# Optimization experiments

Measured on AMD Instinct MI355X. Metric: run time of the kernel, lower is better.

## Reference

```python
import jax, jax.numpy as jnp
import numpy as np
import math

B, C, IMG, P = 32, 3, 224, 16
E, DEPTH, H, MLP = 768, 12, 12, 3072
NP = (IMG // P) ** 2          # 196 patches
S = NP + 1                    # 197 tokens with cls
NCLS = 10
HD = E // H                   # 64 head dim
EPS = 1e-5


def setup_inputs() -> dict:
    key = jax.random.key(0)
    ks = iter(jax.random.split(key, 64))
    n = lambda shape, s=0.02: (jax.random.normal(next(ks), shape, jnp.float32) * s)
    inp = {
        "x": jax.random.normal(next(ks), (B, C, IMG, IMG), jnp.float32),
        "conv_w": n((E, C, P, P)),
        "conv_b": jnp.zeros((E,), jnp.float32),
        "cls_token": n((1, 1, E)),
        "pos_embed": n((1, S, E)),
        # stacked per-layer params, leading dim DEPTH; linear weights stored [in, out]
        "ln1_w": jnp.ones((DEPTH, E), jnp.float32),
        "ln1_b": jnp.zeros((DEPTH, E), jnp.float32),
        "qkv_w": n((DEPTH, E, 3 * E)),
        "qkv_b": jnp.zeros((DEPTH, 3 * E), jnp.float32),
        "proj_w": n((DEPTH, E, E)),
        "proj_b": jnp.zeros((DEPTH, E), jnp.float32),
        "ln2_w": jnp.ones((DEPTH, E), jnp.float32),
        "ln2_b": jnp.zeros((DEPTH, E), jnp.float32),
        "mlp_w1": n((DEPTH, E, MLP)),
        "mlp_b1": jnp.zeros((DEPTH, MLP), jnp.float32),
        "mlp_w2": n((DEPTH, MLP, E)),
        "mlp_b2": jnp.zeros((DEPTH, E), jnp.float32),
        "lnf_w": jnp.ones((E,), jnp.float32),
        "lnf_b": jnp.zeros((E,), jnp.float32),
        "head_w": n((E, NCLS)),
        "head_b": jnp.zeros((NCLS,), jnp.float32),
    }
    return inp


def layernorm(x, w, b):
    mu = jnp.mean(x, axis=-1, keepdims=True)
    var = jnp.mean(jnp.square(x - mu), axis=-1, keepdims=True)
    return (x - mu) * jax.lax.rsqrt(var + EPS) * w + b


def reference(x, conv_w, conv_b, cls_token, pos_embed,
              ln1_w, ln1_b, qkv_w, qkv_b, proj_w, proj_b,
              ln2_w, ln2_b, mlp_w1, mlp_b1, mlp_w2, mlp_b2,
              lnf_w, lnf_b, head_w, head_b):
    # --- patch embedding: stride-P, kernel-P conv == patchify + matmul ---
    g = IMG // P  # 14
    patches = x.reshape(B, C, g, P, g, P).transpose(0, 2, 4, 1, 3, 5).reshape(B, NP, C * P * P)
    wp = conv_w.reshape(E, C * P * P)
    tok = jnp.einsum('bpd,ed->bpe', patches, wp) + conv_b  # [B, NP, E]

    # cls token + positional embedding (dropout = identity at eval)
    h = jnp.concatenate([jnp.broadcast_to(cls_token, (B, 1, E)), tok], axis=1) + pos_embed

    scale = math.sqrt(HD)
    for i in range(DEPTH):
        # --- attention ---
        y = layernorm(h, ln1_w[i], ln1_b[i])
        qkv = (y @ qkv_w[i] + qkv_b[i]).reshape(B, S, 3, H, HD)
        q, k, v = qkv[:, :, 0], qkv[:, :, 1], qkv[:, :, 2]  # [B, S, H, HD]
        attn = jnp.einsum('bqhd,bkhd->bhqk', q, k) / scale
        attn = jax.nn.softmax(attn, axis=-1)
        o = jnp.einsum('bhqk,bkhd->bqhd', attn, v).reshape(B, S, E)
        h = h + (o @ proj_w[i] + proj_b[i])
        # --- MLP ---
        y = layernorm(h, ln2_w[i], ln2_b[i])
        y = jax.nn.gelu(y @ mlp_w1[i] + mlp_b1[i], approximate=False)
        h = h + (y @ mlp_w2[i] + mlp_b2[i])

    h = layernorm(h, lnf_w, lnf_b)
    return h[:, 0] @ head_w + head_b  # [B, NCLS]
```

## Files before the change

### kernel.cpp

```cpp
#include <hip/hip_runtime.h>


typedef __attribute__((ext_vector_type(8))) short short8;
typedef __attribute__((ext_vector_type(8))) unsigned short ushort8;
typedef __attribute__((ext_vector_type(4))) float f32x4;
typedef unsigned short u16;

#define DEV __device__ __forceinline__

DEV u16 f2bf(float f) {
  unsigned int u = __builtin_bit_cast(unsigned int, f);
  u += 0x7fffu + ((u >> 16) & 1u);
  return (u16)(u >> 16);
}
DEV float bf2f(u16 v) {
  return __builtin_bit_cast(float, (unsigned int)v << 16);
}
DEV float wred_sum(float v) {
  for (int o = 32; o; o >>= 1) v += __shfl_xor(v, o, 64);
  return v;
}
DEV void glds16(const void* gp, void* lp) {
  __builtin_amdgcn_global_load_lds(
      (const __attribute__((address_space(1))) void*)gp,
      (__attribute__((address_space(3))) void*)lp, 16, 0, 0);
}
DEV int xcd_swz(int flat, int nwg) {
  int q = nwg >> 3, r = nwg & 7;
  int x = flat & 7, o = flat >> 3;
  return (x < r ? x * (q + 1) : r * (q + 1) + (x - r) * q) + o;
}

__global__ __launch_bounds__(256) void cvt4_k(const float* __restrict__ s,
                                              u16* __restrict__ d, long n4) {
  long i = (long)blockIdx.x * 256 + threadIdx.x;
  if (i >= n4) return;
  float4 v = ((const float4*)s)[i];
  ushort4 o;
  o.x = f2bf(v.x); o.y = f2bf(v.y); o.z = f2bf(v.z); o.w = f2bf(v.w);
  ((ushort4*)d)[i] = o;
}

__global__ __launch_bounds__(256) void tpose_k(const float* __restrict__ s,
                                               u16* __restrict__ d, int K,
                                               int N) {
  __shared__ float t[32][33];
  const int bx = blockIdx.x;
  const int by = blockIdx.y;
  const size_t base = (size_t)blockIdx.z * K * N;
  const int c = threadIdx.x & 31, r0 = threadIdx.x >> 5;
#pragma unroll
  for (int i = 0; i < 4; ++i) {
    int r = r0 + i * 8;
    t[r][c] = s[base + (size_t)(by * 32 + r) * N + bx * 32 + c];
  }
  __syncthreads();
#pragma unroll
  for (int i = 0; i < 4; ++i) {
    int r = r0 + i * 8;
    d[base + (size_t)(bx * 32 + r) * K + by * 32 + c] = f2bf(t[c][r]);
  }
}

__global__ __launch_bounds__(256) void patch_k(const float* __restrict__ x,
                                               u16* __restrict__ pt) {
  int i = blockIdx.x * 256 + threadIdx.x;
  int d = i % 768;
  int bp = i / 768;
  int p = bp % 196, b = bp / 196;
  int c = d >> 8, pd = d & 255;
  int py = pd >> 4, px = pd & 15;
  int gy = p / 14, gx = p - gy * 14;
  size_t src = ((size_t)(b * 3 + c) * 224 + gy * 16 + py) * 224 + gx * 16 + px;
  pt[i] = f2bf(x[src]);
}

__global__ __launch_bounds__(256) void clspos_k(const float* __restrict__ cls,
                                                const float* __restrict__ pos,
                                                float* __restrict__ h) {
  int i = blockIdx.x * 256 + threadIdx.x;
  int b = i / 768, e = i - b * 768;
  h[(size_t)b * 197 * 768 + e] = cls[e] + pos[e];
}

template <int EPI>
DEV void epi_store(float v, int grow, int gcol, u16* outb, int ldo,
                   float* outf, const float* pos) {
  if constexpr (EPI == 0) {
    outb[(size_t)grow * ldo + gcol] = f2bf(v);
  } else if constexpr (EPI == 1) {
    float u = __expf(-1.5957691216f * (v + 0.044715f * v * v * v));
    outb[(size_t)grow * ldo + gcol] = f2bf(v / (1.f + u));
  } else if constexpr (EPI == 2) {
    outf[(size_t)grow * ldo + gcol] += v;
  } else {
    int b = grow / 196, p = grow - b * 196;
    outf[(size_t)(grow + b + 1) * 768 + gcol] =
        v + pos[(size_t)(p + 1) * 768 + gcol];
  }
}

template <int EPI>
__global__ __launch_bounds__(512) void gemmK64(
    const u16* __restrict__ A, int lda, const u16* __restrict__ Bt, int ldb,
    const float* __restrict__ bias, u16* __restrict__ outb, int ldo,
    float* __restrict__ outf, const float* __restrict__ pos, int M, int N,
    int K) {
  __shared__ __align__(16) u16 Ak[2][128 * 64];
  __shared__ __align__(16) u16 Bk[2][128 * 64];
  const int tid = threadIdx.x;
  const int lane = tid & 63, wid = tid >> 6;
  const int wm = wid >> 2, wn = wid & 3;
  const int lg = lane >> 4, lr = lane & 15;
  const int nwg = gridDim.x * gridDim.y;
  const int wg = xcd_swz(blockIdx.y * gridDim.x + blockIdx.x, nwg);
  const int tn = wg % gridDim.x, tm = wg / gridDim.x;

  const int r8 = lane >> 3, c8 = lane & 7;
  const int swc = (c8 ^ r8) << 3;
  const u16* aS = A + (size_t)(tm * 128 + wid * 16 + r8) * lda + swc;
  const u16* bS = Bt + (size_t)(tn * 128 + wid * 16 + r8) * ldb + swc;

  auto stage = [&](int buf, int kt) {
    const u16* ak = aS + kt * 64;
    const u16* bk = bS + kt * 64;
    u16* ad = &Ak[buf][wid * 1024];
    u16* bd = &Bk[buf][wid * 1024];
    glds16(ak, ad);
    glds16(ak + (size_t)8 * lda, ad + 512);
    glds16(bk, bd);
    glds16(bk + (size_t)8 * ldb, bd + 512);
  };

  f32x4 acc[4][2] = {};
  auto compute = [&](int buf) {
#pragma unroll
    for (int ks = 0; ks < 2; ++ks) {
      const int pc = (ks << 2) | lg;
      const int po = ((pc ^ (lr & 7)) << 3);
      short8 af[4], bf2[2];
#pragma unroll
      for (int i = 0; i < 4; ++i)
        af[i] = *(const short8*)(&Ak[buf][(wm * 64 + i * 16 + lr) * 64 + po]);
#pragma unroll
      for (int i = 0; i < 2; ++i)
        bf2[i] = *(const short8*)(&Bk[buf][(wn * 32 + i * 16 + lr) * 64 + po]);
#pragma unroll
      for (int mi = 0; mi < 4; ++mi)
#pragma unroll
        for (int ni = 0; ni < 2; ++ni)
          acc[mi][ni] = __builtin_amdgcn_mfma_f32_16x16x32_bf16(
              af[mi], bf2[ni], acc[mi][ni], 0, 0, 0);
    }
  };

  const int nk = K >> 6;
  int cur = 0;
  stage(0, 0);
  __syncthreads();
  for (int kt = 0; kt < nk - 1; ++kt) {
    stage(cur ^ 1, kt + 1);
    compute(cur);
    __syncthreads();
    cur ^= 1;
  }
  compute(cur);

#pragma unroll
  for (int mi = 0; mi < 4; ++mi)
#pragma unroll
    for (int ni = 0; ni < 2; ++ni)
#pragma unroll
      for (int r = 0; r < 4; ++r) {
        int grow = tm * 128 + wm * 64 + mi * 16 + lg * 4 + r;
        int gcol = tn * 128 + wn * 32 + ni * 16 + lr;
        if (grow < M)
          epi_store<EPI>(acc[mi][ni][r] + bias[gcol], grow, gcol, outb, ldo,
                         outf, pos);
      }
}

template <int EPI>
__global__ __launch_bounds__(512) void gemmW2(
    const u16* __restrict__ A, int lda, const u16* __restrict__ Bt, int ldb,
    const float* __restrict__ bias, u16* __restrict__ outb, int ldo,
    float* __restrict__ outf, int M, int K) {
  __shared__ __align__(16) u16 Ak[2][128 * 32];
  __shared__ __align__(16) u16 Bk[2][256 * 32];
  const int tid = threadIdx.x;
  const int lane = tid & 63, wid = tid >> 6;
  const int wm = wid >> 2, wn = wid & 3;
  const int lg = lane >> 4, lr = lane & 15;
  const int nwg = gridDim.x * gridDim.y;
  const int wg = xcd_swz(blockIdx.y * gridDim.x + blockIdx.x, nwg);
  const int tn = wg % gridDim.x, tm = wg / gridDim.x;
  const size_t koff = (EPI == 4) ? (size_t)blockIdx.z * K : 0;

  const int sr = lane >> 2;
  const int sc4 = (((lane & 3) ^ ((lane >> 3) & 3)) << 3);
  const u16* aSrc = A + (size_t)(tm * 128 + wid * 16 + sr) * lda + koff + sc4;
  const u16* bSrc = Bt + (size_t)(tn * 256 + wid * 32 + sr) * ldb + koff + sc4;
  const size_t bRow16 = (size_t)16 * ldb;

  auto stage = [&](int buf, int kt) {
    const u16* ak = aSrc + kt * 32;
    const u16* bk = bSrc + kt * 32;
    glds16(ak, &Ak[buf][wid * 16 * 32]);
    u16* bd = &Bk[buf][wid * 32 * 32];
    glds16(bk, bd);
    glds16(bk + bRow16, bd + 512);
  };

  const int rp = (lg ^ ((lr >> 1) & 3)) << 3;
  f32x4 acc[4][4] = {};
  auto compute = [&](int buf) {
    short8 af[4], bf[4];
#pragma unroll
    for (int i = 0; i < 4; ++i)
      af[i] = *(const short8*)(&Ak[buf][(wm * 64 + i * 16 + lr) * 32 + rp]);
#pragma unroll
    for (int i = 0; i < 4; ++i)
      bf[i] = *(const short8*)(&Bk[buf][(wn * 64 + i * 16 + lr) * 32 + rp]);
#pragma unroll
    for (int mi = 0; mi < 4; ++mi)
#pragma unroll
      for (int ni = 0; ni < 4; ++ni)
        acc[mi][ni] = __builtin_amdgcn_mfma_f32_16x16x32_bf16(
            af[mi], bf[ni], acc[mi][ni], 0, 0, 0);
  };

  const int nk = K >> 5;
  int cur = 0;
  stage(0, 0);
  __syncthreads();
  for (int kt = 0; kt < nk - 1; ++kt) {
    stage(cur ^ 1, kt + 1);
    compute(cur);
    __syncthreads();
    cur ^= 1;
  }
  compute(cur);

#pragma unroll
  for (int mi = 0; mi < 4; ++mi)
#pragma unroll
    for (int ni = 0; ni < 4; ++ni)
#pragma unroll
      for (int r = 0; r < 4; ++r) {
        int grow = tm * 128 + wm * 64 + mi * 16 + lg * 4 + r;
        int gcol = tn * 256 + wn * 64 + ni * 16 + lr;
        if (grow < M) {
          if constexpr (EPI == 4) {
            outb[(size_t)blockIdx.z * M * ldo + (size_t)grow * ldo + gcol] =
                f2bf(acc[mi][ni][r]);
          } else {
            epi_store<EPI>(acc[mi][ni][r] + bias[gcol], grow, gcol, outb, ldo,
                           outf, nullptr);
          }
        }
      }
}

__global__ __launch_bounds__(256) void redK(const u16* __restrict__ Cp,
                                            const float* __restrict__ bias,
                                            float* __restrict__ h) {
  size_t i = ((size_t)blockIdx.x * 256 + threadIdx.x) * 4;
  ushort4 q0 = *(const ushort4*)(Cp + i);
  ushort4 q1 = *(const ushort4*)(Cp + 6304ull * 768 + i);
  ushort4 q2 = *(const ushort4*)(Cp + 2ull * 6304 * 768 + i);
  float4 hv = *(const float4*)(h + i);
  float4 bv = *(const float4*)(bias + (int)(i % 768));
  hv.x += bf2f(q0.x) + bf2f(q1.x) + bf2f(q2.x) + bv.x;
  hv.y += bf2f(q0.y) + bf2f(q1.y) + bf2f(q2.y) + bv.y;
  hv.z += bf2f(q0.z) + bf2f(q1.z) + bf2f(q2.z) + bv.z;
  hv.w += bf2f(q0.w) + bf2f(q1.w) + bf2f(q2.w) + bv.w;
  *(float4*)(h + i) = hv;
}

__global__ __launch_bounds__(256) void redln_k(
    const u16* __restrict__ Cp, const float* __restrict__ bias,
    float* __restrict__ h, const float* __restrict__ lnw,
    const float* __restrict__ lnb, u16* __restrict__ y) {
  const int lane = threadIdx.x & 63, wv = threadIdx.x >> 6;
  const int r = blockIdx.x * 4 + wv;
  const size_t base = (size_t)r * 768;
  float4 a[3];
  float s = 0.f, q = 0.f;
#pragma unroll
  for (int i = 0; i < 3; ++i) {
    const int off = i * 256 + lane * 4;
    float4 hv = *(const float4*)(h + base + off);
    ushort4 q0 = *(const ushort4*)(Cp + base + off);
    ushort4 q1 = *(const ushort4*)(Cp + 6304ull * 768 + base + off);
    ushort4 q2 = *(const ushort4*)(Cp + 2ull * 6304 * 768 + base + off);
    float4 bv = *(const float4*)(bias + off);
    a[i].x = hv.x + bf2f(q0.x) + bf2f(q1.x) + bf2f(q2.x) + bv.x;
    a[i].y = hv.y + bf2f(q0.y) + bf2f(q1.y) + bf2f(q2.y) + bv.y;
    a[i].z = hv.z + bf2f(q0.z) + bf2f(q1.z) + bf2f(q2.z) + bv.z;
    a[i].w = hv.w + bf2f(q0.w) + bf2f(q1.w) + bf2f(q2.w) + bv.w;
    s += a[i].x + a[i].y + a[i].z + a[i].w;
    q += a[i].x * a[i].x + a[i].y * a[i].y + a[i].z * a[i].z +
         a[i].w * a[i].w;
  }
  s = wred_sum(s);
  q = wred_sum(q);
  float mu = s * (1.f / 768.f);
  float var = q * (1.f / 768.f) - mu * mu;
  float rs = rsqrtf(var + 1e-5f);
#pragma unroll
  for (int i = 0; i < 3; ++i) {
    const int off = i * 256 + lane * 4;
    *(float4*)(h + base + off) = a[i];
    float4 wv4 = *(const float4*)(lnw + off);
    float4 bv4 = *(const float4*)(lnb + off);
    ushort4 o;
    o.x = f2bf((a[i].x - mu) * rs * wv4.x + bv4.x);
    o.y = f2bf((a[i].y - mu) * rs * wv4.y + bv4.y);
    o.z = f2bf((a[i].z - mu) * rs * wv4.z + bv4.z);
    o.w = f2bf((a[i].w - mu) * rs * wv4.w + bv4.w);
    *(ushort4*)(y + base + off) = o;
  }
}

template <int EPI, int BM>
__global__ __launch_bounds__(256) void gemmP(
    const u16* __restrict__ A, int lda, const u16* __restrict__ Bt, int ldb,
    const float* __restrict__ bias, u16* __restrict__ outb, int ldo,
    float* __restrict__ outf, const float* __restrict__ pos, int M, int N,
    int K) {
  constexpr int MI = BM / 32;
  __shared__ __align__(16) u16 Ak[2][BM * 32];
  __shared__ __align__(16) u16 Bk[2][128 * 32];
  const int tid = threadIdx.x;
  const int lane = tid & 63, wid = tid >> 6;
  const int wm = wid >> 1, wn = wid & 1;
  const int lg = lane >> 4, lr = lane & 15;
  const int nwg = gridDim.x * gridDim.y;
  const int wg = xcd_swz(blockIdx.y * gridDim.x + blockIdx.x, nwg);
  const int tn = wg % gridDim.x, tm = wg / gridDim.x;

  const int sr = lane >> 2;
  const int sc4 = (((lane & 3) ^ ((lane >> 3) & 3)) << 3);
  const u16* aSrc = A + (size_t)(tm * BM + wid * (BM / 4) + sr) * lda + sc4;
  const u16* bSrc = Bt + (size_t)(tn * 128 + wid * 32 + sr) * ldb + sc4;
  const size_t aRow16 = (size_t)16 * lda, bRow16 = (size_t)16 * ldb;

  auto stage = [&](int buf, int kt) {
    const u16* ak = aSrc + kt * 32;
    const u16* bk = bSrc + kt * 32;
    u16* ad = &Ak[buf][wid * (BM / 4) * 32];
    u16* bd = &Bk[buf][wid * 1024];
    glds16(ak, ad);
    if constexpr (BM == 128) glds16(ak + aRow16, ad + 512);
    glds16(bk, bd);
    glds16(bk + bRow16, bd + 512);
  };

  const int rp = (lg ^ ((lr >> 1) & 3)) << 3;
  f32x4 acc[MI][4] = {};
  auto compute = [&](int buf) {
    short8 af[MI], bfr[4];
#pragma unroll
    for (int i = 0; i < MI; ++i)
      af[i] =
          *(const short8*)(&Ak[buf][(wm * (BM / 2) + i * 16 + lr) * 32 + rp]);
#pragma unroll
    for (int i = 0; i < 4; ++i)
      bfr[i] = *(const short8*)(&Bk[buf][(wn * 64 + i * 16 + lr) * 32 + rp]);
#pragma unroll
    for (int mi = 0; mi < MI; ++mi)
#pragma unroll
      for (int ni = 0; ni < 4; ++ni)
        acc[mi][ni] = __builtin_amdgcn_mfma_f32_16x16x32_bf16(
            af[mi], bfr[ni], acc[mi][ni], 0, 0, 0);
  };

  const int nk = K >> 5;
  int cur = 0;
  stage(0, 0);
  __syncthreads();
  for (int kt = 0; kt < nk - 1; ++kt) {
    stage(cur ^ 1, kt + 1);
    compute(cur);
    __syncthreads();
    cur ^= 1;
  }
  compute(cur);

#pragma unroll
  for (int mi = 0; mi < MI; ++mi)
#pragma unroll
    for (int ni = 0; ni < 4; ++ni)
#pragma unroll
      for (int r = 0; r < 4; ++r) {
        int grow = tm * BM + wm * (BM / 2) + mi * 16 + lg * 4 + r;
        int gcol = tn * 128 + wn * 64 + ni * 16 + lr;
        if (grow < M)
          epi_store<EPI>(acc[mi][ni][r] + bias[gcol], grow, gcol, outb, ldo,
                         outf, pos);
      }
}

__global__ __launch_bounds__(256) void qksm_k(const u16* __restrict__ qkv,
                                              u16* __restrict__ P) {
  __shared__ __align__(16) u16 Ks[224 * 64];
  const int bh = blockIdx.x;
  const int tid = threadIdx.x;
  const int lane = tid & 63, w = tid >> 6;
  const int lg = lane >> 4, lr = lane & 15;
  const int b = bh / 12, hh = bh - b * 12;
  const u16* kbase = qkv + (size_t)b * 197 * 2304 + 768 + hh * 64;
#pragma unroll
  for (int it = 0; it < 7; ++it) {
    const int c0 = it * 256 + w * 64;
    const int c = c0 + lane;
    const int rd = c >> 3, c8 = c & 7;
    const int rc = rd > 196 ? 196 : rd;
    glds16(kbase + (size_t)rc * 2304 + ((c8 ^ (rd & 7)) << 3), &Ks[c0 * 8]);
  }
  __syncthreads();

  const u16* base = qkv + (size_t)b * 197 * 2304 + hh * 64;
  const bool kval12 = (12 * 16 + lr) <= 196;
  for (int qt = w; qt < 13; qt += 4) {
    int qrow = qt * 16 + lr;
    if (qrow > 196) qrow = 196;
    const u16* qp = base + (size_t)qrow * 2304 + lg * 8;
    short8 a0 = *(const short8*)(qp);
    short8 a1 = *(const short8*)(qp + 32);
    f32x4 c[13];
#pragma unroll
    for (int kt = 0; kt < 13; ++kt) {
      const int krow = kt * 16 + lr;
      short8 b0 =
          *(const short8*)(&Ks[krow * 64 + ((lg ^ (krow & 7)) << 3)]);
      short8 b1 =
          *(const short8*)(&Ks[krow * 64 + (((4 + lg) ^ (krow & 7)) << 3)]);
      f32x4 t = {0.f, 0.f, 0.f, 0.f};
      t = __builtin_amdgcn_mfma_f32_16x16x32_bf16(a0, b0, t, 0, 0, 0);
      c[kt] = __builtin_amdgcn_mfma_f32_16x16x32_bf16(a1, b1, t, 0, 0, 0);
    }
    float mr[4], sr_[4];
#pragma unroll
    for (int r = 0; r < 4; ++r) {
      float mm = -3.4e38f;
#pragma unroll
      for (int kt = 0; kt < 13; ++kt)
        if (kt < 12 || kval12) mm = fmaxf(mm, c[kt][r] * 0.125f);
#pragma unroll
      for (int o = 1; o < 16; o <<= 1) mm = fmaxf(mm, __shfl_xor(mm, o, 64));
      mr[r] = mm;
    }
#pragma unroll
    for (int r = 0; r < 4; ++r) {
      float s = 0.f;
#pragma unroll
      for (int kt = 0; kt < 13; ++kt) {
        float e =
            (kt < 12 || kval12) ? __expf(c[kt][r] * 0.125f - mr[r]) : 0.f;
        c[kt][r] = e;
        s += e;
      }
#pragma unroll
      for (int o = 1; o < 16; o <<= 1) s += __shfl_xor(s, o, 64);
      sr_[r] = 1.0f / s;
    }
    u16* pb = P + (size_t)bh * 197 * 224;
#pragma unroll
    for (int r = 0; r < 4; ++r) {
      int q = qt * 16 + lg * 4 + r;
      if (q < 197) {
#pragma unroll
        for (int kt = 0; kt < 13; ++kt)
          pb[(size_t)q * 224 + kt * 16 + lr] = f2bf(c[kt][r] * sr_[r]);
        pb[(size_t)q * 224 + 208 + lr] = 0;
      }
    }
  }
}

__global__ __launch_bounds__(256) void pv_k(const u16* __restrict__ qkv,
                                            const u16* __restrict__ P,
                                            u16* __restrict__ o) {
  __shared__ __align__(16) u16 Vs[224 * 64];
  const int bh = blockIdx.x;
  const int b = bh / 12, hh = bh - b * 12;
  const int tid = threadIdx.x;
  const int lane = tid & 63, ct = tid >> 6;
  const int lg = lane >> 4, lr = lane & 15;
  const u16* vhead = qkv + (size_t)b * 197 * 2304 + 1536 + hh * 64;
#pragma unroll
  for (int it = 0; it < 7; ++it) {
    const int c0 = it * 256 + ct * 64;
    const int c = c0 + lane;
    int row = c >> 3;
    if (row > 196) row = 196;
    glds16(vhead + (size_t)row * 2304 + (c & 7) * 8, &Vs[c0 * 8]);
  }
  __syncthreads();
  short8 vf[7];
#pragma unroll
  for (int ks = 0; ks < 7; ++ks) {
    ushort8 t;
#pragma unroll
    for (int j = 0; j < 8; ++j) {
      int kk = ks * 32 + lg * 8 + j;
      t[j] = Vs[kk * 64 + ct * 16 + lr];
    }
    vf[ks] = __builtin_bit_cast(short8, t);
  }
  const u16* pbase = P + (size_t)bh * 197 * 224;
  u16* ob = o + (size_t)b * 197 * 768 + hh * 64 + ct * 16;
  for (int qt = 0; qt < 13; ++qt) {
    int q = qt * 16 + lr;
    if (q > 196) q = 196;
    const u16* pp = pbase + (size_t)q * 224 + lg * 8;
    f32x4 acc = {0.f, 0.f, 0.f, 0.f};
#pragma unroll
    for (int ks = 0; ks < 7; ++ks) {
      short8 af = *(const short8*)(pp + ks * 32);
      acc = __builtin_amdgcn_mfma_f32_16x16x32_bf16(af, vf[ks], acc, 0, 0, 0);
    }
#pragma unroll
    for (int r = 0; r < 4; ++r) {
      int qq = qt * 16 + lg * 4 + r;
      if (qq < 197) ob[(size_t)qq * 768 + lr] = f2bf(acc[r]);
    }
  }
}

__global__ __launch_bounds__(256) void ln_k(const float* __restrict__ x,
                                            const float* __restrict__ w,
                                            const float* __restrict__ bb,
                                            u16* __restrict__ y) {
  const int lane = threadIdx.x & 63, wv = threadIdx.x >> 6;
  const int r = blockIdx.x * 4 + wv;
  const float* xr = x + (size_t)r * 768;
  float4 v[3];
  float s = 0.f, q = 0.f;
#pragma unroll
  for (int i = 0; i < 3; ++i) {
    v[i] = *(const float4*)(xr + i * 256 + lane * 4);
    s += v[i].x + v[i].y + v[i].z + v[i].w;
    q += v[i].x * v[i].x + v[i].y * v[i].y + v[i].z * v[i].z +
         v[i].w * v[i].w;
  }
  s = wred_sum(s);
  q = wred_sum(q);
  float mu = s * (1.f / 768.f);
  float var = q * (1.f / 768.f) - mu * mu;
  float rs = rsqrtf(var + 1e-5f);
  u16* yr = y + (size_t)r * 768;
#pragma unroll
  for (int i = 0; i < 3; ++i) {
    float4 wv4 = *(const float4*)(w + i * 256 + lane * 4);
    float4 bv4 = *(const float4*)(bb + i * 256 + lane * 4);
    ushort4 o;
    o.x = f2bf((v[i].x - mu) * rs * wv4.x + bv4.x);
    o.y = f2bf((v[i].y - mu) * rs * wv4.y + bv4.y);
    o.z = f2bf((v[i].z - mu) * rs * wv4.z + bv4.z);
    o.w = f2bf((v[i].w - mu) * rs * wv4.w + bv4.w);
    *(ushort4*)(yr + i * 256 + lane * 4) = o;
  }
}

__global__ __launch_bounds__(256) void head_k(
    const float* __restrict__ h, const float* __restrict__ lnw,
    const float* __restrict__ lnb, const float* __restrict__ hw,
    const float* __restrict__ hb, float* __restrict__ out) {
  const int b = blockIdx.x, tid = threadIdx.x;
  const float* xr = h + (size_t)b * 197 * 768;
  float v0 = xr[tid], v1 = xr[tid + 256], v2 = xr[tid + 512];
  float s = v0 + v1 + v2;
  float q = v0 * v0 + v1 * v1 + v2 * v2;
  s = wred_sum(s);
  q = wred_sum(q);
  __shared__ float ss[4], qs[4];
  int lane = tid & 63, wid = tid >> 6;
  if (lane == 0) { ss[wid] = s; qs[wid] = q; }
  __syncthreads();
  float S = ss[0] + ss[1] + ss[2] + ss[3];
  float Q = qs[0] + qs[1] + qs[2] + qs[3];
  float mu = S * (1.f / 768.f);
  float var = Q * (1.f / 768.f) - mu * mu;
  float rs = rsqrtf(var + 1e-5f);
  __shared__ float yb[768];
  yb[tid] = (v0 - mu) * rs * lnw[tid] + lnb[tid];
  yb[tid + 256] = (v1 - mu) * rs * lnw[tid + 256] + lnb[tid + 256];
  yb[tid + 512] = (v2 - mu) * rs * lnw[tid + 512] + lnb[tid + 512];
  __syncthreads();
  float p[10] = {};
  for (int e = tid; e < 768; e += 256) {
    float yv = yb[e];
#pragma unroll
    for (int n = 0; n < 10; ++n) p[n] += yv * hw[(size_t)e * 10 + n];
  }
#pragma unroll
  for (int n = 0; n < 10; ++n) p[n] = wred_sum(p[n]);
  __shared__ float red[4][10];
  if (lane == 0)
#pragma unroll
    for (int n = 0; n < 10; ++n) red[wid][n] = p[n];
  __syncthreads();
  if (tid < 10)
    out[b * 10 + tid] =
        red[0][tid] + red[1][tid] + red[2][tid] + red[3][tid] + hb[tid];
}

extern "C" void kernel_launch(void* const* d_in, const int* in_sizes, int n_in,
                              void* d_out, int out_size, void* d_ws,
                              size_t ws_size, hipStream_t stream) {
  const float* x = (const float*)d_in[0];
  const float* conv_w = (const float*)d_in[1];
  const float* conv_b = (const float*)d_in[2];
  const float* cls = (const float*)d_in[3];
  const float* pos = (const float*)d_in[4];
  const float* ln1w = (const float*)d_in[5];
  const float* ln1b = (const float*)d_in[6];
  const float* qkvw = (const float*)d_in[7];
  const float* qkvbias = (const float*)d_in[8];
  const float* projw = (const float*)d_in[9];
  const float* projb = (const float*)d_in[10];
  const float* ln2w = (const float*)d_in[11];
  const float* ln2b = (const float*)d_in[12];
  const float* w1f = (const float*)d_in[13];
  const float* b1 = (const float*)d_in[14];
  const float* w2f = (const float*)d_in[15];
  const float* b2 = (const float*)d_in[16];
  const float* lnfw = (const float*)d_in[17];
  const float* lnfb = (const float*)d_in[18];
  const float* headw = (const float*)d_in[19];
  const float* headb = (const float*)d_in[20];
  float* out = (float*)d_out;

  char* p = (char*)d_ws;
  auto take = [&](size_t bytes) {
    char* q = p;
    p += (bytes + 255) & ~(size_t)255;
    return q;
  };
  u16* wq = (u16*)take(12ull * 768 * 2304 * 2);
  u16* wpj = (u16*)take(12ull * 768 * 768 * 2);
  u16* w1 = (u16*)take(12ull * 768 * 3072 * 2);
  u16* w2 = (u16*)take(12ull * 3072 * 768 * 2);
  u16* wc = (u16*)take(768ull * 768 * 2);
  float* h = (float*)take(6304ull * 768 * 4);
  u16* y = (u16*)take(6400ull * 768 * 2);
  u16* qkv = (u16*)take(6400ull * 2304 * 2);
  u16* ob = (u16*)take(6400ull * 768 * 2);
  u16* mlpb = (u16*)take(6400ull * 3072 * 2);
  u16* P = (u16*)take(384ull * 197 * 224 * 2);
  u16* skPb = (u16*)take(3ull * 6304 * 768 * 2);
  (void)ws_size; (void)in_sizes; (void)n_in; (void)out_size;

  tpose_k<<<dim3(72, 24, 12), 256, 0, stream>>>(qkvw, wq, 768, 2304);
  tpose_k<<<dim3(24, 24, 12), 256, 0, stream>>>(projw, wpj, 768, 768);
  tpose_k<<<dim3(96, 24, 12), 256, 0, stream>>>(w1f, w1, 768, 3072);
  tpose_k<<<dim3(24, 96, 12), 256, 0, stream>>>(w2f, w2, 3072, 768);
  cvt4_k<<<576, 256, 0, stream>>>(conv_w, wc, 768 * 768 / 4);

  patch_k<<<6272 * 768 / 256, 256, 0, stream>>>(x, mlpb);
  gemmP<3, 64><<<dim3(6, 98), 256, 0, stream>>>(mlpb, 768, wc, 768, conv_b,
                                                nullptr, 0, h, pos, 6272, 768,
                                                768);
  clspos_k<<<32 * 768 / 256, 256, 0, stream>>>(cls, pos, h);

  ln_k<<<1576, 256, 0, stream>>>(h, ln1w, ln1b, y);
  for (int i = 0; i < 12; ++i) {
    gemmW2<0><<<dim3(9, 50), 512, 0, stream>>>(
        y, 768, wq + (size_t)i * 768 * 2304, 768, qkvbias + i * 2304, qkv,
        2304, nullptr, 6304, 768);
    qksm_k<<<384, 256, 0, stream>>>(qkv, P);
    pv_k<<<384, 256, 0, stream>>>(qkv, P, ob);
    gemmP<2, 64><<<dim3(6, 99), 256, 0, stream>>>(
        ob, 768, wpj + (size_t)i * 768 * 768, 768, projb + i * 768, nullptr,
        768, h, nullptr, 6304, 768, 768);
    ln_k<<<1576, 256, 0, stream>>>(h, ln2w + i * 768, ln2b + i * 768, y);
    gemmK64<1><<<dim3(24, 50), 512, 0, stream>>>(
        y, 768, w1 + (size_t)i * 768 * 3072, 768, b1 + i * 3072, mlpb, 3072,
        nullptr, nullptr, 6304, 3072, 768);
    gemmW2<4><<<dim3(3, 50, 3), 512, 0, stream>>>(
        mlpb, 3072, w2 + (size_t)i * 3072 * 768, 3072, nullptr, skPb, 768,
        nullptr, 6304, 1024);
    if (i < 11) {
      redln_k<<<1576, 256, 0, stream>>>(skPb, b2 + i * 768, h,
                                        ln1w + (i + 1) * 768,
                                        ln1b + (i + 1) * 768, y);
    } else {
      redK<<<4728, 256, 0, stream>>>(skPb, b2 + i * 768, h);
    }
  }

  head_k<<<32, 256, 0, stream>>>(h, lnfw, lnfb, headw, headb, out);
}
```

Measured before the change: 2.841 ms.

## Fuse QK-softmax and PV attention kernels, keeping probabilities in LDS

Merges the two attention kernels into one per-(batch,head) kernel. It loads both K and V into shared memory, computes the softmax probabilities per query tile into a per-wave LDS buffer, then immediately multiplies by V held in registers. This removes the global round trip of the P matrix and one launch per layer. In exchange it raises LDS use per block and register pressure, since each wave now holds all of V's fragments, which may lower occupancy.

```diff
diff --git a/kernel.cpp b/kernel.cpp
--- a/kernel.cpp
+++ b/kernel.cpp
@@ -401,39 +401,66 @@
       }
 }
 
-__global__ __launch_bounds__(256) void qksm_k(const u16* __restrict__ qkv,
-                                              u16* __restrict__ P) {
-  __shared__ __align__(16) u16 Ks[224 * 64];
+__global__ __launch_bounds__(256) void attn_k(const u16* __restrict__ qkv,
+                                              u16* __restrict__ o) {
+  __shared__ __align__(16) u16 Ks[208 * 64];
+  __shared__ __align__(16) u16 Vs[224 * 64];
+  __shared__ __align__(16) u16 Ps[4][16 * 208];
   const int bh = blockIdx.x;
   const int tid = threadIdx.x;
   const int lane = tid & 63, w = tid >> 6;
   const int lg = lane >> 4, lr = lane & 15;
   const int b = bh / 12, hh = bh - b * 12;
   const u16* kbase = qkv + (size_t)b * 197 * 2304 + 768 + hh * 64;
+  const u16* vbase = kbase + 768;
+#pragma unroll
+  for (int it = 0; it < 7; ++it) {
+    const int c0 = it * 256 + w * 64;
+    if (c0 < 1664) {
+      const int c = c0 + lane;
+      const int rd = c >> 3, c8 = c & 7;
+      const int rc = rd > 196 ? 196 : rd;
+      glds16(kbase + (size_t)rc * 2304 + ((c8 ^ (rd & 7)) << 3), &Ks[c0 * 8]);
+    }
+  }
 #pragma unroll
   for (int it = 0; it < 7; ++it) {
     const int c0 = it * 256 + w * 64;
     const int c = c0 + lane;
-    const int rd = c >> 3, c8 = c & 7;
-    const int rc = rd > 196 ? 196 : rd;
-    glds16(kbase + (size_t)rc * 2304 + ((c8 ^ (rd & 7)) << 3), &Ks[c0 * 8]);
-  }
-  __syncthreads();
-
-  const u16* base = qkv + (size_t)b * 197 * 2304 + hh * 64;
-  const bool kval12 = (12 * 16 + lr) <= 196;
+    int row = c >> 3;
+    if (row > 196) row = 196;
+    glds16(vbase + (size_t)row * 2304 + (c & 7) * 8, &Vs[c0 * 8]);
+  }
+  __syncthreads();
+
+  short8 vf[7][4];
+#pragma unroll
+  for (int ks = 0; ks < 7; ++ks)
+#pragma unroll
+    for (int ct = 0; ct < 4; ++ct) {
+      ushort8 t;
+#pragma unroll
+      for (int j = 0; j < 8; ++j)
+        t[j] = Vs[(ks * 32 + lg * 8 + j) * 64 + ct * 16 + lr];
+      vf[ks][ct] = __builtin_bit_cast(short8, t);
+    }
+
+  const u16* qb = qkv + (size_t)b * 197 * 2304 + hh * 64;
+  u16* ob = o + (size_t)b * 197 * 768 + hh * 64;
+  u16* Pw = &Ps[w][0];
+  const bool kval12 = (192 + lr) <= 196;
+  const short8 zf = {};
   for (int qt = w; qt < 13; qt += 4) {
     int qrow = qt * 16 + lr;
     if (qrow > 196) qrow = 196;
-    const u16* qp = base + (size_t)qrow * 2304 + lg * 8;
+    const u16* qp = qb + (size_t)qrow * 2304 + lg * 8;
     short8 a0 = *(const short8*)(qp);
     short8 a1 = *(const short8*)(qp + 32);
     f32x4 c[13];
 #pragma unroll
     for (int kt = 0; kt < 13; ++kt) {
       const int krow = kt * 16 + lr;
-      short8 b0 =
-          *(const short8*)(&Ks[krow * 64 + ((lg ^ (krow & 7)) << 3)]);
+      short8 b0 = *(const short8*)(&Ks[krow * 64 + ((lg ^ (krow & 7)) << 3)]);
       short8 b1 =
           *(const short8*)(&Ks[krow * 64 + (((4 + lg) ^ (krow & 7)) << 3)]);
       f32x4 t = {0.f, 0.f, 0.f, 0.f};
@@ -448,7 +475,8 @@
       for (int kt = 0; kt < 13; ++kt)
         if (kt < 12 || kval12) mm = fmaxf(mm, c[kt][r] * 0.125f);
 #pragma unroll
-      for (int o = 1; o < 16; o <<= 1) mm = fmaxf(mm, __shfl_xor(mm, o, 64));
+      for (int oo = 1; oo < 16; oo <<= 1)
+        mm = fmaxf(mm, __shfl_xor(mm, oo, 64));
       mr[r] = mm;
     }
 #pragma unroll
@@ -462,70 +490,38 @@
         s += e;
       }
 #pragma unroll
-      for (int o = 1; o < 16; o <<= 1) s += __shfl_xor(s, o, 64);
+      for (int oo = 1; oo < 16; oo <<= 1) s += __shfl_xor(s, oo, 64);
       sr_[r] = 1.0f / s;
     }
-    u16* pb = P + (size_t)bh * 197 * 224;
-#pragma unroll
-    for (int r = 0; r < 4; ++r) {
-      int q = qt * 16 + lg * 4 + r;
-      if (q < 197) {
-#pragma unroll
-        for (int kt = 0; kt < 13; ++kt)
-          pb[(size_t)q * 224 + kt * 16 + lr] = f2bf(c[kt][r] * sr_[r]);
-        pb[(size_t)q * 224 + 208 + lr] = 0;
+#pragma unroll
+    for (int r = 0; r < 4; ++r)
+#pragma unroll
+      for (int kt = 0; kt < 13; ++kt)
+        Pw[(lg * 4 + r) * 208 + kt * 16 + lr] = f2bf(c[kt][r] * sr_[r]);
+    asm volatile("s_waitcnt lgkmcnt(0)" ::: "memory");
+    __builtin_amdgcn_sched_barrier(0);
+    f32x4 acc[4] = {};
+#pragma unroll
+    for (int ks = 0; ks < 7; ++ks) {
+      short8 af;
+      if (ks == 6 && lg >= 2) {
+        af = zf;
+      } else {
+        af = *(const short8*)(Pw + lr * 208 + ks * 32 + lg * 8);
       }
-    }
-  }
-}
-
-__global__ __launch_bounds__(256) void pv_k(const u16* __restrict__ qkv,
-                                            const u16* __restrict__ P,
-                                            u16* __restrict__ o) {
-  __shared__ __align__(16) u16 Vs[224 * 64];
-  const int bh = blockIdx.x;
-  const int b = bh / 12, hh = bh - b * 12;
-  const int tid = threadIdx.x;
-  const int lane = tid & 63, ct = tid >> 6;
-  const int lg = lane >> 4, lr = lane & 15;
-  const u16* vhead = qkv + (size_t)b * 197 * 2304 + 1536 + hh * 64;
-#pragma unroll
-  for (int it = 0; it < 7; ++it) {
-    const int c0 = it * 256 + ct * 64;
-    const int c = c0 + lane;
-    int row = c >> 3;
-    if (row > 196) row = 196;
-    glds16(vhead + (size_t)row * 2304 + (c & 7) * 8, &Vs[c0 * 8]);
-  }
-  __syncthreads();
-  short8 vf[7];
-#pragma unroll
-  for (int ks = 0; ks < 7; ++ks) {
-    ushort8 t;
-#pragma unroll
-    for (int j = 0; j < 8; ++j) {
-      int kk = ks * 32 + lg * 8 + j;
-      t[j] = Vs[kk * 64 + ct * 16 + lr];
-    }
-    vf[ks] = __builtin_bit_cast(short8, t);
-  }
-  const u16* pbase = P + (size_t)bh * 197 * 224;
-  u16* ob = o + (size_t)b * 197 * 768 + hh * 64 + ct * 16;
-  for (int qt = 0; qt < 13; ++qt) {
-    int q = qt * 16 + lr;
-    if (q > 196) q = 196;
-    const u16* pp = pbase + (size_t)q * 224 + lg * 8;
-    f32x4 acc = {0.f, 0.f, 0.f, 0.f};
-#pragma unroll
-    for (int ks = 0; ks < 7; ++ks) {
-      short8 af = *(const short8*)(pp + ks * 32);
-      acc = __builtin_amdgcn_mfma_f32_16x16x32_bf16(af, vf[ks], acc, 0, 0, 0);
-    }
-#pragma unroll
-    for (int r = 0; r < 4; ++r) {
-      int qq = qt * 16 + lg * 4 + r;
-      if (qq < 197) ob[(size_t)qq * 768 + lr] = f2bf(acc[r]);
-    }
+#pragma unroll
+      for (int ct = 0; ct < 4; ++ct)
+        acc[ct] =
+            __builtin_amdgcn_mfma_f32_16x16x32_bf16(af, vf[ks][ct], acc[ct],
+                                                    0, 0, 0);
+    }
+#pragma unroll
+    for (int ct = 0; ct < 4; ++ct)
+#pragma unroll
+      for (int r = 0; r < 4; ++r) {
+        int qq = qt * 16 + lg * 4 + r;
+        if (qq < 197) ob[(size_t)qq * 768 + ct * 16 + lr] = f2bf(acc[ct][r]);
+      }
   }
 }
 
@@ -649,7 +645,6 @@
   u16* qkv = (u16*)take(6400ull * 2304 * 2);
   u16* ob = (u16*)take(6400ull * 768 * 2);
   u16* mlpb = (u16*)take(6400ull * 3072 * 2);
-  u16* P = (u16*)take(384ull * 197 * 224 * 2);
   u16* skPb = (u16*)take(3ull * 6304 * 768 * 2);
   (void)ws_size; (void)in_sizes; (void)n_in; (void)out_size;
 
@@ -670,8 +665,7 @@
     gemmW2<0><<<dim3(9, 50), 512, 0, stream>>>(
         y, 768, wq + (size_t)i * 768 * 2304, 768, qkvbias + i * 2304, qkv,
         2304, nullptr, 6304, 768);
-    qksm_k<<<384, 256, 0, stream>>>(qkv, P);
-    pv_k<<<384, 256, 0, stream>>>(qkv, P, ob);
+    attn_k<<<384, 256, 0, stream>>>(qkv, ob);
     gemmP<2, 64><<<dim3(6, 99), 256, 0, stream>>>(
         ob, 768, wpj + (size_t)i * 768 * 768, 768, projb + i * 768, nullptr,
         768, h, nullptr, 6304, 768, 768);
```

New measurement: 2.788 ms. About the same (-1.9%).
